# Kernel optimization log

Hardware: AMD Instinct MI355X
Metric: run time of the kernel (lower is better)

The kernel has to match this reference:

```python
import jax, jax.numpy as jnp
import numpy as np

N, E, G = 100000, 3200000, 128
F, H = 9, 64


def _lin(key, fan_in, fan_out):
    s = 1.0 / np.sqrt(fan_in)
    k1, k2 = jax.random.split(key)
    W = jax.random.uniform(k1, (fan_in, fan_out), minval=-s, maxval=s, dtype=jnp.float32)
    b = jax.random.uniform(k2, (fan_out,), minval=-s, maxval=s, dtype=jnp.float32)
    return W, b


def setup_inputs() -> dict:
    key = jax.random.key(0)
    ks = jax.random.split(key, 16)
    x = jax.random.normal(ks[0], (N, F), dtype=jnp.float32)
    edge_index = jax.random.randint(ks[1], (2, E), 0, N, dtype=jnp.int64)
    edge_attr = jax.random.normal(ks[2], (E, 1), dtype=jnp.float32)
    batch = jnp.sort(jax.random.randint(ks[3], (N,), 0, G, dtype=jnp.int64))
    B_total = jax.random.uniform(ks[4], (G,), dtype=jnp.float32)
    terminal_mask = jax.random.randint(ks[5], (N,), 0, 2, dtype=jnp.int32)
    c_cost = jax.random.uniform(ks[6], (N,), dtype=jnp.float32)
    We1, be1 = _lin(ks[7], 1, F)   # GINEConv edge projection edge_dim->in_channels
    W1a, b1a = _lin(ks[8], F, H)
    W1b, b1b = _lin(ks[9], H, H)
    We2, be2 = _lin(ks[10], 1, H)
    W2a, b2a = _lin(ks[11], H, H)
    W2b, b2b = _lin(ks[12], H, H)
    Wr1, br1 = _lin(ks[13], H, H // 2)
    Wr2, br2 = _lin(ks[14], H // 2, 1)
    return dict(x=x, edge_index=edge_index, edge_attr=edge_attr, batch=batch,
                B_total=B_total, terminal_mask=terminal_mask, c_cost=c_cost,
                We1=We1, be1=be1, W1a=W1a, b1a=b1a, W1b=W1b, b1b=b1b,
                We2=We2, be2=be2, W2a=W2a, b2a=b2a, W2b=W2b, b2b=b2b,
                Wr1=Wr1, br1=br1, Wr2=Wr2, br2=br2)


def _gine_conv(h, src, dst, edge_attr, We, be, Wa, ba, Wb, bb):
    # GINEConv (eps=0): nn((1+eps)*x_i + sum_j ReLU(x_j + Lin(edge_attr)))
    ea = edge_attr @ We + be                      # [E, dim]
    msg = jax.nn.relu(h[src] + ea)                # gather + edge fuse + relu
    agg = jax.ops.segment_sum(msg, dst, num_segments=N)  # scatter-add
    z = h + agg
    z = jax.nn.relu(z @ Wa + ba)
    return jax.nn.relu(z @ Wb + bb)


def reference(x, edge_index, edge_attr, batch, B_total, terminal_mask, c_cost,
              We1, be1, W1a, b1a, W1b, b1b, We2, be2, W2a, b2a, W2b, b2b,
              Wr1, br1, Wr2, br2):
    src, dst = edge_index[0], edge_index[1]
    h = _gine_conv(x, src, dst, edge_attr, We1, be1, W1a, b1a, W1b, b1b)
    h = _gine_conv(h, src, dst, edge_attr, We2, be2, W2a, b2a, W2b, b2b)
    pi_raw = jax.nn.sigmoid(jax.nn.relu(h @ Wr1 + br1) @ Wr2 + br2)[:, 0]  # [N]
    pi_raw = pi_raw * (1.0 - terminal_mask.astype(pi_raw.dtype))
    node_expenses = pi_raw * c_cost
    total_expenses = jax.ops.segment_sum(node_expenses, batch, num_segments=B_total.shape[0])
    ratio = jnp.minimum(B_total[batch] / (total_expenses[batch] + 1e-12), 1.0)
    return pi_raw * ratio
```

## Files before the change

### kernel.cpp

```cpp
#include <hip/hip_runtime.h>
#include <hip/hip_fp16.h>
#include <math.h>

#define TPB 256
#define P_BLOCKS 512
#define BSHIFT 8
#define BINS_MAX 512

struct alignas(8)  h2x2 { __half2 a, b; };
struct alignas(16) h2x4 { __half2 a, b, c, d; };

typedef _Float16 f16;
typedef __attribute__((ext_vector_type(8))) _Float16 f16x8;
typedef __attribute__((ext_vector_type(4))) float f32x4;

#define MFMA16(a, b, c) __builtin_amdgcn_mfma_f32_16x16x32_f16(a, b, c, 0, 0, 0)

__global__ void __launch_bounds__(256) k_bhist(const int* __restrict__ dst,
                                               int* __restrict__ counts, int E, int B) {
  __shared__ int h[BINS_MAX];
  int t = threadIdx.x, blk = blockIdx.x;
  for (int i = t; i < B; i += TPB) h[i] = 0;
  __syncthreads();
  int chunk = (E + P_BLOCKS - 1) / P_BLOCKS;
  int s = blk * chunk, e = min(E, s + chunk);
  for (int i = s + t; i < e; i += TPB)
    atomicAdd(&h[__builtin_nontemporal_load(&dst[i]) >> BSHIFT], 1);
  __syncthreads();
  for (int i = t; i < B; i += TPB) counts[i * P_BLOCKS + blk] = h[i];
}

__global__ void k_scan_block(const int* __restrict__ deg, int* __restrict__ offs,
                             int* __restrict__ bsums, int n) {
  __shared__ int lds[256];
  int t = threadIdx.x, b = blockIdx.x;
  int base = b * 1024 + t * 4;
  int v0 = (base + 0 < n) ? deg[base + 0] : 0;
  int v1 = (base + 1 < n) ? deg[base + 1] : 0;
  int v2 = (base + 2 < n) ? deg[base + 2] : 0;
  int v3 = (base + 3 < n) ? deg[base + 3] : 0;
  int s = v0 + v1 + v2 + v3;
  lds[t] = s;
  __syncthreads();
  int acc = s;
  for (int off = 1; off < 256; off <<= 1) {
    int x = (t >= off) ? lds[t - off] : 0;
    __syncthreads();
    acc += x;
    lds[t] = acc;
    __syncthreads();
  }
  int excl = acc - s;
  if (base + 0 < n) offs[base + 0] = excl;
  if (base + 1 < n) offs[base + 1] = excl + v0;
  if (base + 2 < n) offs[base + 2] = excl + v0 + v1;
  if (base + 3 < n) offs[base + 3] = excl + v0 + v1 + v2;
  if (t == 255) bsums[b] = acc;
}

__global__ void k_scan_mid(int* __restrict__ bsums, int nb) {
  __shared__ int lds[256];
  int t = threadIdx.x;
  int v = (t < nb) ? bsums[t] : 0;
  lds[t] = v;
  __syncthreads();
  int acc = v;
  for (int off = 1; off < 256; off <<= 1) {
    int x = (t >= off) ? lds[t - off] : 0;
    __syncthreads();
    acc += x;
    lds[t] = acc;
    __syncthreads();
  }
  if (t < nb) bsums[t] = acc - v;
}

__global__ void k_scan_add(int* __restrict__ offs, const int* __restrict__ bsums,
                           int n, int total) {
  int t = threadIdx.x, b = blockIdx.x;
  int add = bsums[b];
  int base = b * 1024 + t * 4;
#pragma unroll
  for (int j = 0; j < 4; ++j)
    if (base + j < n) offs[base + j] += add;
  if (b == 0 && t == 0) offs[n] = total;
}

__global__ void __launch_bounds__(256) k_bfill(const int* __restrict__ src,
                                               const int* __restrict__ dst,
                                               const float* __restrict__ attr,
                                               const int* __restrict__ offs,
                                               int2* __restrict__ ebuf, int E, int B) {
  __shared__ int cur[BINS_MAX];
  int t = threadIdx.x, blk = blockIdx.x;
  for (int i = t; i < B; i += TPB) cur[i] = offs[i * P_BLOCKS + blk];
  __syncthreads();
  int chunk = (E + P_BLOCKS - 1) / P_BLOCKS;
  int s = blk * chunk, e = min(E, s + chunk);
#pragma unroll 4
  for (int i = s + t; i < e; i += TPB) {
    int d = __builtin_nontemporal_load(&dst[i]);
    int sv = __builtin_nontemporal_load(&src[i]);
    float av = __builtin_nontemporal_load(&attr[i]);
    int bin = d >> BSHIFT;
    int pos = atomicAdd(&cur[bin], 1);
    ebuf[pos] = make_int2((sv << BSHIFT) | (d & ((1 << BSHIFT) - 1)), __float_as_int(av));
  }
}

__global__ void __launch_bounds__(256) k_bsort(const long long* __restrict__ ebuf,
                                               const int* __restrict__ offs,
                                               int2* __restrict__ csr,
                                               int* __restrict__ noffs,
                                               int N, int E) {
  __shared__ int hist[256];
  __shared__ int cursor[256];
  __shared__ int sc[256];
  int t = threadIdx.x, bkt = blockIdx.x;
  hist[t] = 0;
  __syncthreads();
  int s = offs[bkt * P_BLOCKS], e = offs[(bkt + 1) * P_BLOCKS];
#pragma unroll 4
  for (int i = s + t; i < e; i += TPB) {
    long long pv = __builtin_nontemporal_load(&ebuf[i]);
    int key = (int)(unsigned int)(pv & 0xffffffffLL);
    atomicAdd(&hist[key & 255], 1);
  }
  __syncthreads();
  int v = hist[t];
  int acc = v;
  sc[t] = v;
  __syncthreads();
  for (int off = 1; off < 256; off <<= 1) {
    int x = (t >= off) ? sc[t - off] : 0;
    __syncthreads();
    acc += x;
    sc[t] = acc;
    __syncthreads();
  }
  int base = s + acc - v;
  cursor[t] = base;
  int n = (bkt << BSHIFT) + t;
  if (n < N) noffs[n] = base;
  if (bkt == 0 && t == 0) noffs[N] = E;
  __syncthreads();
#pragma unroll 4
  for (int i = s + t; i < e; i += TPB) {
    long long pv = __builtin_nontemporal_load(&ebuf[i]);
    int key = (int)(unsigned int)(pv & 0xffffffffLL);
    int attr = (int)(unsigned int)(((unsigned long long)pv) >> 32);
    int pos = atomicAdd(&cursor[key & 255], 1);
    csr[pos] = make_int2(((unsigned int)key) >> BSHIFT, attr);
  }
}

__global__ void __launch_bounds__(256) k_agg1(
    const float* __restrict__ x, const int2* __restrict__ csr,
    const int* __restrict__ noffs, const float* __restrict__ We1,
    const float* __restrict__ be1, float* __restrict__ u1, int N) {
  int t = blockIdx.x * TPB + threadIdx.x;
  int node = t >> 4, f = t & 15;
  if (node >= N || f >= 9) return;
  int o0 = noffs[node], o1 = noffs[node + 1];
  float we = We1[f], be = be1[f];
  float acc = 0.f;
  int last = o1 - 1;
  for (int e = o0; e < o1; e += 8) {
    int i0 = e;     bool m0 = i0 < o1; i0 = m0 ? i0 : last;
    int i1 = e + 1; bool m1 = i1 < o1; i1 = m1 ? i1 : last;
    int i2 = e + 2; bool m2 = i2 < o1; i2 = m2 ? i2 : last;
    int i3 = e + 3; bool m3 = i3 < o1; i3 = m3 ? i3 : last;
    int i4 = e + 4; bool m4 = i4 < o1; i4 = m4 ? i4 : last;
    int i5 = e + 5; bool m5 = i5 < o1; i5 = m5 ? i5 : last;
    int i6 = e + 6; bool m6 = i6 < o1; i6 = m6 ? i6 : last;
    int i7 = e + 7; bool m7 = i7 < o1; i7 = m7 ? i7 : last;
    int2 p0 = csr[i0], p1 = csr[i1], p2 = csr[i2], p3 = csr[i3];
    int2 p4 = csr[i4], p5 = csr[i5], p6 = csr[i6], p7 = csr[i7];
    float v0 = x[p0.x * 9 + f] + fmaf(__int_as_float(p0.y), we, be);
    float v1 = x[p1.x * 9 + f] + fmaf(__int_as_float(p1.y), we, be);
    float v2 = x[p2.x * 9 + f] + fmaf(__int_as_float(p2.y), we, be);
    float v3 = x[p3.x * 9 + f] + fmaf(__int_as_float(p3.y), we, be);
    float v4 = x[p4.x * 9 + f] + fmaf(__int_as_float(p4.y), we, be);
    float v5 = x[p5.x * 9 + f] + fmaf(__int_as_float(p5.y), we, be);
    float v6 = x[p6.x * 9 + f] + fmaf(__int_as_float(p6.y), we, be);
    float v7 = x[p7.x * 9 + f] + fmaf(__int_as_float(p7.y), we, be);
    acc += m0 ? fmaxf(v0, 0.f) : 0.f;
    acc += m1 ? fmaxf(v1, 0.f) : 0.f;
    acc += m2 ? fmaxf(v2, 0.f) : 0.f;
    acc += m3 ? fmaxf(v3, 0.f) : 0.f;
    acc += m4 ? fmaxf(v4, 0.f) : 0.f;
    acc += m5 ? fmaxf(v5, 0.f) : 0.f;
    acc += m6 ? fmaxf(v6, 0.f) : 0.f;
    acc += m7 ? fmaxf(v7, 0.f) : 0.f;
  }
  u1[node * 9 + f] = x[node * 9 + f] + acc;
}

__global__ void __launch_bounds__(256) k_agg2(
    const __half* __restrict__ h1, const long long* __restrict__ csr,
    const int* __restrict__ noffs, const float* __restrict__ We2,
    const float* __restrict__ be2, float* __restrict__ u2, int N) {
  int gt = blockIdx.x * TPB + threadIdx.x;
  int node = gt >> 6;
  if (node >= N) return;
  int lane = gt & 63;
  int q = lane >> 3, c = lane & 7;
  float4 weA = *(const float4*)&We2[c * 8];
  float4 weB = *(const float4*)&We2[c * 8 + 4];
  float4 beA = *(const float4*)&be2[c * 8];
  float4 beB = *(const float4*)&be2[c * 8 + 4];
  int o0 = noffs[node], o1 = noffs[node + 1];
  float a0 = 0.f, a1 = 0.f, a2 = 0.f, a3 = 0.f, a4 = 0.f, a5 = 0.f, a6 = 0.f, a7 = 0.f;

#define AGG2_ACCM(pv, v, m)                                                  \
  {                                                                          \
    float ea = __int_as_float((int)(unsigned int)(((unsigned long long)(pv)) >> 32)); \
    float2 f0 = __half22float2((v).a), f1 = __half22float2((v).b);           \
    float2 f2 = __half22float2((v).c), f3 = __half22float2((v).d);           \
    a0 += (m) ? fmaxf(f0.x + fmaf(ea, weA.x, beA.x), 0.f) : 0.f;             \
    a1 += (m) ? fmaxf(f0.y + fmaf(ea, weA.y, beA.y), 0.f) : 0.f;             \
    a2 += (m) ? fmaxf(f1.x + fmaf(ea, weA.z, beA.z), 0.f) : 0.f;             \
    a3 += (m) ? fmaxf(f1.y + fmaf(ea, weA.w, beA.w), 0.f) : 0.f;             \
    a4 += (m) ? fmaxf(f2.x + fmaf(ea, weB.x, beB.x), 0.f) : 0.f;             \
    a5 += (m) ? fmaxf(f2.y + fmaf(ea, weB.y, beB.y), 0.f) : 0.f;             \
    a6 += (m) ? fmaxf(f3.x + fmaf(ea, weB.z, beB.z), 0.f) : 0.f;             \
    a7 += (m) ? fmaxf(f3.y + fmaf(ea, weB.w, beB.w), 0.f) : 0.f;             \
  }

  int e = o0;
  if (o1 - e > 32) {
    int last = o1 - 1;
    do {
      long long pv0, pv1, pv2, pv3, pv4, pv5, pv6, pv7;
      bool m0, m1, m2, m3, m4, m5, m6, m7;
      {
        int i0 = e + q;      m0 = i0 < o1; i0 = m0 ? i0 : last;
        int i1 = e + 8 + q;  m1 = i1 < o1; i1 = m1 ? i1 : last;
        int i2 = e + 16 + q; m2 = i2 < o1; i2 = m2 ? i2 : last;
        int i3 = e + 24 + q; m3 = i3 < o1; i3 = m3 ? i3 : last;
        int i4 = e + 32 + q; m4 = i4 < o1; i4 = m4 ? i4 : last;
        int i5 = e + 40 + q; m5 = i5 < o1; i5 = m5 ? i5 : last;
        int i6 = e + 48 + q; m6 = i6 < o1; i6 = m6 ? i6 : last;
        int i7 = e + 56 + q; m7 = i7 < o1; i7 = m7 ? i7 : last;
        pv0 = __builtin_nontemporal_load(&csr[i0]);
        pv1 = __builtin_nontemporal_load(&csr[i1]);
        pv2 = __builtin_nontemporal_load(&csr[i2]);
        pv3 = __builtin_nontemporal_load(&csr[i3]);
        pv4 = __builtin_nontemporal_load(&csr[i4]);
        pv5 = __builtin_nontemporal_load(&csr[i5]);
        pv6 = __builtin_nontemporal_load(&csr[i6]);
        pv7 = __builtin_nontemporal_load(&csr[i7]);
      }
      h2x4 v0 = *(const h2x4*)(h1 + (size_t)(int)(unsigned int)(pv0 & 0xffffffffLL) * 64 + c * 8);
      h2x4 v1 = *(const h2x4*)(h1 + (size_t)(int)(unsigned int)(pv1 & 0xffffffffLL) * 64 + c * 8);
      h2x4 v2 = *(const h2x4*)(h1 + (size_t)(int)(unsigned int)(pv2 & 0xffffffffLL) * 64 + c * 8);
      h2x4 v3 = *(const h2x4*)(h1 + (size_t)(int)(unsigned int)(pv3 & 0xffffffffLL) * 64 + c * 8);
      h2x4 v4 = *(const h2x4*)(h1 + (size_t)(int)(unsigned int)(pv4 & 0xffffffffLL) * 64 + c * 8);
      h2x4 v5 = *(const h2x4*)(h1 + (size_t)(int)(unsigned int)(pv5 & 0xffffffffLL) * 64 + c * 8);
      h2x4 v6 = *(const h2x4*)(h1 + (size_t)(int)(unsigned int)(pv6 & 0xffffffffLL) * 64 + c * 8);
      h2x4 v7 = *(const h2x4*)(h1 + (size_t)(int)(unsigned int)(pv7 & 0xffffffffLL) * 64 + c * 8);
      AGG2_ACCM(pv0, v0, m0); AGG2_ACCM(pv1, v1, m1);
      AGG2_ACCM(pv2, v2, m2); AGG2_ACCM(pv3, v3, m3);
      AGG2_ACCM(pv4, v4, m4); AGG2_ACCM(pv5, v5, m5);
      AGG2_ACCM(pv6, v6, m6); AGG2_ACCM(pv7, v7, m7);
      e += 64;
    } while (o1 - e > 32);
  }
  if (e < o1) {
    int last = o1 - 1;
    int i0 = e + q;      bool m0 = i0 < o1; i0 = m0 ? i0 : last;
    int i1 = e + 8 + q;  bool m1 = i1 < o1; i1 = m1 ? i1 : last;
    int i2 = e + 16 + q; bool m2 = i2 < o1; i2 = m2 ? i2 : last;
    int i3 = e + 24 + q; bool m3 = i3 < o1; i3 = m3 ? i3 : last;
    long long pv0 = __builtin_nontemporal_load(&csr[i0]);
    long long pv1 = __builtin_nontemporal_load(&csr[i1]);
    long long pv2 = __builtin_nontemporal_load(&csr[i2]);
    long long pv3 = __builtin_nontemporal_load(&csr[i3]);
    h2x4 v0 = *(const h2x4*)(h1 + (size_t)(int)(unsigned int)(pv0 & 0xffffffffLL) * 64 + c * 8);
    h2x4 v1 = *(const h2x4*)(h1 + (size_t)(int)(unsigned int)(pv1 & 0xffffffffLL) * 64 + c * 8);
    h2x4 v2 = *(const h2x4*)(h1 + (size_t)(int)(unsigned int)(pv2 & 0xffffffffLL) * 64 + c * 8);
    h2x4 v3 = *(const h2x4*)(h1 + (size_t)(int)(unsigned int)(pv3 & 0xffffffffLL) * 64 + c * 8);
    AGG2_ACCM(pv0, v0, m0); AGG2_ACCM(pv1, v1, m1);
    AGG2_ACCM(pv2, v2, m2); AGG2_ACCM(pv3, v3, m3);
  }
#undef AGG2_ACCM

  a0 += __shfl_xor(a0, 8, 64); a0 += __shfl_xor(a0, 16, 64); a0 += __shfl_xor(a0, 32, 64);
  a1 += __shfl_xor(a1, 8, 64); a1 += __shfl_xor(a1, 16, 64); a1 += __shfl_xor(a1, 32, 64);
  a2 += __shfl_xor(a2, 8, 64); a2 += __shfl_xor(a2, 16, 64); a2 += __shfl_xor(a2, 32, 64);
  a3 += __shfl_xor(a3, 8, 64); a3 += __shfl_xor(a3, 16, 64); a3 += __shfl_xor(a3, 32, 64);
  a4 += __shfl_xor(a4, 8, 64); a4 += __shfl_xor(a4, 16, 64); a4 += __shfl_xor(a4, 32, 64);
  a5 += __shfl_xor(a5, 8, 64); a5 += __shfl_xor(a5, 16, 64); a5 += __shfl_xor(a5, 32, 64);
  a6 += __shfl_xor(a6, 8, 64); a6 += __shfl_xor(a6, 16, 64); a6 += __shfl_xor(a6, 32, 64);
  a7 += __shfl_xor(a7, 8, 64); a7 += __shfl_xor(a7, 16, 64); a7 += __shfl_xor(a7, 32, 64);

  if (q == 0) {
    h2x4 sf = *(const h2x4*)(h1 + (size_t)node * 64 + c * 8);
    float2 s0 = __half22float2(sf.a), s1 = __half22float2(sf.b);
    float2 s2 = __half22float2(sf.c), s3 = __half22float2(sf.d);
    float4 oA, oB;
    oA.x = s0.x + a0; oA.y = s0.y + a1; oA.z = s1.x + a2; oA.w = s1.y + a3;
    oB.x = s2.x + a4; oB.y = s2.y + a5; oB.z = s3.x + a6; oB.w = s3.y + a7;
    *(float4*)&u2[(size_t)node * 64 + c * 8] = oA;
    *(float4*)&u2[(size_t)node * 64 + c * 8 + 4] = oB;
  }
}

__device__ __forceinline__ void splitf8(const float* v, f16x8& h, f16x8& l) {
#pragma unroll
  for (int j = 0; j < 8; ++j) {
    float x = v[j];
    f16 hh = (f16)x;
    h[j] = hh;
    l[j] = (f16)(x - (float)hh);
  }
}

__device__ __forceinline__ void pack_w(const float* __restrict__ W, int Ntiles, int nslots,
                                       f16* hi, f16* lo, int t) {
  int lane = t & 63;
  int kg = lane >> 4, m = lane & 15;
  int Nout = Ntiles * 16;
  for (int s = t >> 6; s < nslots; s += 4) {
    int ks = s / Ntiles, nt = s - ks * Ntiles;
    int kbase = ks * 32 + kg * 8;
    int n = nt * 16 + m;
    float v[8];
#pragma unroll
    for (int j = 0; j < 8; ++j) v[j] = W[(kbase + j) * Nout + n];
    f16x8 h, l;
    splitf8(v, h, l);
    *(f16x8*)&hi[(s * 64 + lane) * 8] = h;
    *(f16x8*)&lo[(s * 64 + lane) * 8] = l;
  }
}

__global__ void __launch_bounds__(256) k_mlp9(
    const float* __restrict__ uin, const float* __restrict__ Wa,
    const float* __restrict__ ba, const float* __restrict__ Wb,
    const float* __restrict__ bb, __half* __restrict__ hout, int N) {
  __shared__ __align__(16) f16 wf1h[2048], wf1l[2048];
  __shared__ __align__(16) f16 wf2h[4096], wf2l[4096];
  __shared__ float ls_z[64 * 65];
  __shared__ float ls_ba[64], ls_bb[64];
  const int t = threadIdx.x;
  const int n0 = blockIdx.x * 64;
  const int w = t >> 6, lane = t & 63;
  const int m = lane & 15, kg = lane >> 4;

  {
    int s = w;
    int n = s * 16 + m;
    float v[8];
#pragma unroll
    for (int j = 0; j < 8; ++j) {
      int k = kg * 8 + j;
      v[j] = (k < 9) ? Wa[k * 64 + n] : 0.f;
    }
    f16x8 h, l;
    splitf8(v, h, l);
    *(f16x8*)&wf1h[(s * 64 + lane) * 8] = h;
    *(f16x8*)&wf1l[(s * 64 + lane) * 8] = l;
  }
  pack_w(Wb, 4, 8, wf2h, wf2l, t);
  if (t < 64) { ls_ba[t] = ba[t]; ls_bb[t] = bb[t]; }
  __syncthreads();

  int row = min(n0 + w * 16 + m, N - 1);
  float av[8];
#pragma unroll
  for (int j = 0; j < 8; ++j) {
    int k = kg * 8 + j;
    av[j] = (k < 9) ? uin[(size_t)row * 9 + k] : 0.f;
  }
  f16x8 a0h, a0l, a1h, a1l;
  splitf8(av, a0h, a0l);

  f32x4 acc[4];
#pragma unroll
  for (int nt = 0; nt < 4; ++nt) { f32x4 z4 = {0.f, 0.f, 0.f, 0.f}; acc[nt] = z4; }
#pragma unroll
  for (int nt = 0; nt < 4; ++nt) {
    f16x8 bh = *(const f16x8*)&wf1h[(nt * 64 + lane) * 8];
    f16x8 bl = *(const f16x8*)&wf1l[(nt * 64 + lane) * 8];
    acc[nt] = MFMA16(a0h, bh, acc[nt]);
    acc[nt] = MFMA16(a0l, bh, acc[nt]);
    acc[nt] = MFMA16(a0h, bl, acc[nt]);
  }
#pragma unroll
  for (int nt = 0; nt < 4; ++nt)
#pragma unroll
    for (int r = 0; r < 4; ++r)
      ls_z[(w * 16 + kg * 4 + r) * 65 + nt * 16 + m] = fmaxf(acc[nt][r] + ls_ba[nt * 16 + m], 0.f);
  __syncthreads();

  const float* zr = &ls_z[(size_t)(w * 16 + m) * 65 + kg * 8];
  {
    float zv0[8], zv1[8];
#pragma unroll
    for (int j = 0; j < 8; ++j) { zv0[j] = zr[j]; zv1[j] = zr[32 + j]; }
    splitf8(zv0, a0h, a0l);
    splitf8(zv1, a1h, a1l);
  }
#pragma unroll
  for (int nt = 0; nt < 4; ++nt) { f32x4 z4 = {0.f, 0.f, 0.f, 0.f}; acc[nt] = z4; }
#pragma unroll
  for (int nt = 0; nt < 4; ++nt) {
#pragma unroll
    for (int ks = 0; ks < 2; ++ks) {
      int s = ks * 4 + nt;
      f16x8 bh = *(const f16x8*)&wf2h[(s * 64 + lane) * 8];
      f16x8 bl = *(const f16x8*)&wf2l[(s * 64 + lane) * 8];
      f16x8 ah = ks ? a1h : a0h;
      f16x8 al = ks ? a1l : a0l;
      acc[nt] = MFMA16(ah, bh, acc[nt]);
      acc[nt] = MFMA16(al, bh, acc[nt]);
      acc[nt] = MFMA16(ah, bl, acc[nt]);
    }
  }
#pragma unroll
  for (int nt = 0; nt < 4; ++nt)
#pragma unroll
    for (int r = 0; r < 4; ++r) {
      int node = n0 + w * 16 + kg * 4 + r;
      if (node < N)
        hout[(size_t)node * 64 + nt * 16 + m] =
            __float2half(fmaxf(acc[nt][r] + ls_bb[nt * 16 + m], 0.f));
    }
}

__global__ void __launch_bounds__(256) k_mlp_ro(
    const float* __restrict__ uin, const float* __restrict__ Wa,
    const float* __restrict__ ba, const float* __restrict__ Wb,
    const float* __restrict__ bb, const float* __restrict__ Wr1,
    const float* __restrict__ br1, const float* __restrict__ Wr2,
    const float* __restrict__ br2, const int* __restrict__ tmask,
    float* __restrict__ pi, int N) {
  __shared__ __align__(16) f16 wf1h[4096], wf1l[4096];
  __shared__ __align__(16) f16 wf2h[4096], wf2l[4096];
  __shared__ __align__(16) f16 wfrh[2048], wfrl[2048];
  __shared__ float ls_z[64 * 65];
  __shared__ float ls_ba[64], ls_bb[64], ls_br1[32], ls_w2[32];
  const int t = threadIdx.x;
  const int n0 = blockIdx.x * 64;

  pack_w(Wa, 4, 8, wf1h, wf1l, t);
  pack_w(Wb, 4, 8, wf2h, wf2l, t);
  pack_w(Wr1, 2, 4, wfrh, wfrl, t);
  if (t < 64) { ls_ba[t] = ba[t]; ls_bb[t] = bb[t]; }
  else if (t < 96) { ls_br1[t - 64] = br1[t - 64]; ls_w2[t - 64] = Wr2[t - 64]; }
  __syncthreads();

  const int w = t >> 6, lane = t & 63;
  const int m = lane & 15, kg = lane >> 4;

  int row = n0 + w * 16 + m;
  row = min(row, N - 1);
  const float* ar = uin + (size_t)row * 64 + kg * 8;
  float av0[8], av1[8];
  {
    f32x4 p0 = *(const f32x4*)ar;
    f32x4 p1 = *(const f32x4*)(ar + 4);
    f32x4 p2 = *(const f32x4*)(ar + 32);
    f32x4 p3 = *(const f32x4*)(ar + 36);
#pragma unroll
    for (int j = 0; j < 4; ++j) {
      av0[j] = p0[j]; av0[4 + j] = p1[j];
      av1[j] = p2[j]; av1[4 + j] = p3[j];
    }
  }
  f16x8 a0h, a0l, a1h, a1l;
  splitf8(av0, a0h, a0l);
  splitf8(av1, a1h, a1l);

  f32x4 acc[4];
#pragma unroll
  for (int nt = 0; nt < 4; ++nt) { f32x4 z4 = {0.f, 0.f, 0.f, 0.f}; acc[nt] = z4; }
#pragma unroll
  for (int nt = 0; nt < 4; ++nt) {
#pragma unroll
    for (int ks = 0; ks < 2; ++ks) {
      int s = ks * 4 + nt;
      f16x8 bh = *(const f16x8*)&wf1h[(s * 64 + lane) * 8];
      f16x8 bl = *(const f16x8*)&wf1l[(s * 64 + lane) * 8];
      f16x8 ah = ks ? a1h : a0h;
      f16x8 al = ks ? a1l : a0l;
      acc[nt] = MFMA16(ah, bh, acc[nt]);
      acc[nt] = MFMA16(al, bh, acc[nt]);
      acc[nt] = MFMA16(ah, bl, acc[nt]);
    }
  }
#pragma unroll
  for (int nt = 0; nt < 4; ++nt)
#pragma unroll
    for (int r = 0; r < 4; ++r)
      ls_z[(w * 16 + kg * 4 + r) * 65 + nt * 16 + m] = fmaxf(acc[nt][r] + ls_ba[nt * 16 + m], 0.f);
  __syncthreads();

  const float* zr = &ls_z[(size_t)(w * 16 + m) * 65 + kg * 8];
  {
    float zv0[8], zv1[8];
#pragma unroll
    for (int j = 0; j < 8; ++j) { zv0[j] = zr[j]; zv1[j] = zr[32 + j]; }
    splitf8(zv0, a0h, a0l);
    splitf8(zv1, a1h, a1l);
  }
#pragma unroll
  for (int nt = 0; nt < 4; ++nt) { f32x4 z4 = {0.f, 0.f, 0.f, 0.f}; acc[nt] = z4; }
#pragma unroll
  for (int nt = 0; nt < 4; ++nt) {
#pragma unroll
    for (int ks = 0; ks < 2; ++ks) {
      int s = ks * 4 + nt;
      f16x8 bh = *(const f16x8*)&wf2h[(s * 64 + lane) * 8];
      f16x8 bl = *(const f16x8*)&wf2l[(s * 64 + lane) * 8];
      f16x8 ah = ks ? a1h : a0h;
      f16x8 al = ks ? a1l : a0l;
      acc[nt] = MFMA16(ah, bh, acc[nt]);
      acc[nt] = MFMA16(al, bh, acc[nt]);
      acc[nt] = MFMA16(ah, bl, acc[nt]);
    }
  }
  __syncthreads();
#pragma unroll
  for (int nt = 0; nt < 4; ++nt)
#pragma unroll
    for (int r = 0; r < 4; ++r)
      ls_z[(w * 16 + kg * 4 + r) * 65 + nt * 16 + m] = fmaxf(acc[nt][r] + ls_bb[nt * 16 + m], 0.f);
  __syncthreads();

  {
    float zv0[8], zv1[8];
#pragma unroll
    for (int j = 0; j < 8; ++j) { zv0[j] = zr[j]; zv1[j] = zr[32 + j]; }
    splitf8(zv0, a0h, a0l);
    splitf8(zv1, a1h, a1l);
  }
  f32x4 accr[2];
#pragma unroll
  for (int nt = 0; nt < 2; ++nt) { f32x4 z4 = {0.f, 0.f, 0.f, 0.f}; accr[nt] = z4; }
#pragma unroll
  for (int nt = 0; nt < 2; ++nt) {
#pragma unroll
    for (int ks = 0; ks < 2; ++ks) {
      int s = ks * 2 + nt;
      f16x8 bh = *(const f16x8*)&wfrh[(s * 64 + lane) * 8];
      f16x8 bl = *(const f16x8*)&wfrl[(s * 64 + lane) * 8];
      f16x8 ah = ks ? a1h : a0h;
      f16x8 al = ks ? a1l : a0l;
      accr[nt] = MFMA16(ah, bh, accr[nt]);
      accr[nt] = MFMA16(al, bh, accr[nt]);
      accr[nt] = MFMA16(ah, bl, accr[nt]);
    }
  }
  float b2 = br2[0];
#pragma unroll
  for (int r = 0; r < 4; ++r) {
    float v0 = fmaxf(accr[0][r] + ls_br1[m], 0.f) * ls_w2[m];
    float v1 = fmaxf(accr[1][r] + ls_br1[16 + m], 0.f) * ls_w2[16 + m];
    float tr = v0 + v1;
    tr += __shfl_xor(tr, 1, 64);
    tr += __shfl_xor(tr, 2, 64);
    tr += __shfl_xor(tr, 4, 64);
    tr += __shfl_xor(tr, 8, 64);
    if (m == 0) {
      int node = n0 + w * 16 + kg * 4 + r;
      if (node < N) {
        float sg = 1.f / (1.f + expf(-(tr + b2)));
        pi[node] = sg * (1.f - (float)tmask[node]);
      }
    }
  }
}

__global__ void k_grpsum(const float* __restrict__ pi, const float* __restrict__ c_cost,
                         const int* __restrict__ batch, float* __restrict__ exp_tot, int N) {
  __shared__ float lsf[256];
  __shared__ int lsi[256];
  int t = threadIdx.x;
  int i = blockIdx.x * TPB + t;
  bool valid = i < N;
  int g = valid ? batch[i] : 0;
  float v = valid ? pi[i] * c_cost[i] : 0.f;
  lsi[t] = valid ? g : 0x7fffffff;
  __syncthreads();
  for (int s = 128; s > 0; s >>= 1) { if (t < s) lsi[t] = min(lsi[t], lsi[t + s]); __syncthreads(); }
  int gmin = lsi[0];
  __syncthreads();
  lsi[t] = valid ? g : -1;
  __syncthreads();
  for (int s = 128; s > 0; s >>= 1) { if (t < s) lsi[t] = max(lsi[t], lsi[t + s]); __syncthreads(); }
  int gmax = lsi[0];
  __syncthreads();
  for (int gg = gmin; gg <= gmax; ++gg) {
    lsf[t] = (valid && g == gg) ? v : 0.f;
    __syncthreads();
    for (int s = 128; s > 0; s >>= 1) { if (t < s) lsf[t] += lsf[t + s]; __syncthreads(); }
    if (t == 0) atomicAdd(&exp_tot[gg], lsf[0]);
    __syncthreads();
  }
}

__global__ void k_final(const float* __restrict__ pi, const int* __restrict__ batch,
                        const float* __restrict__ B_total, const float* __restrict__ exp_tot,
                        float* __restrict__ out, int N) {
  int i = blockIdx.x * TPB + threadIdx.x;
  if (i < N) {
    int g = batch[i];
    float ratio = fminf(B_total[g] / (exp_tot[g] + 1e-12f), 1.f);
    out[i] = pi[i] * ratio;
  }
}

extern "C" void kernel_launch(void* const* d_in, const int* in_sizes, int n_in,
                              void* d_out, int out_size, void* d_ws, size_t ws_size,
                              hipStream_t stream) {
  const float* x     = (const float*)d_in[0];
  const int*   ei    = (const int*)d_in[1];
  const float* eattr = (const float*)d_in[2];
  const int*   batch = (const int*)d_in[3];
  const float* Btot  = (const float*)d_in[4];
  const int*   tmask = (const int*)d_in[5];
  const float* ccost = (const float*)d_in[6];
  const float* We1 = (const float*)d_in[7],  *be1 = (const float*)d_in[8];
  const float* W1a = (const float*)d_in[9],  *b1a = (const float*)d_in[10];
  const float* W1b = (const float*)d_in[11], *b1b = (const float*)d_in[12];
  const float* We2 = (const float*)d_in[13], *be2 = (const float*)d_in[14];
  const float* W2a = (const float*)d_in[15], *b2a = (const float*)d_in[16];
  const float* W2b = (const float*)d_in[17], *b2b = (const float*)d_in[18];
  const float* Wr1 = (const float*)d_in[19], *br1 = (const float*)d_in[20];
  const float* Wr2 = (const float*)d_in[21], *br2 = (const float*)d_in[22];
  float* out = (float*)d_out;

  const int N = in_sizes[0] / 9;
  const int E = in_sizes[2];
  const int G = in_sizes[4];
  const int* src = ei;
  const int* dst = ei + E;
  const int B = (N + (1 << BSHIFT) - 1) >> BSHIFT;
  const int nscan = B * P_BLOCKS;

  size_t cur = 0;
  auto alloc = [&](size_t elems) { size_t r = cur; cur += elems; cur = (cur + 63) & ~(size_t)63; return r; };
  char* wsb = (char*)d_ws;
  size_t o_exp    = alloc(G);
  size_t o_counts = alloc(nscan);
  size_t o_offs   = alloc(nscan + 1);
  size_t o_bsums  = alloc(256);
  size_t o_noffs  = alloc(N + 1);
  size_t o_csr    = alloc(2 * (size_t)E);
  size_t e_or_h   = (2 * (size_t)E > (size_t)N * 32) ? 2 * (size_t)E : (size_t)N * 32;
  size_t o_ebuf   = alloc(e_or_h);
  size_t o_u1     = alloc((size_t)N * 9);
  size_t o_u2     = alloc((size_t)N * 64);
  size_t o_pi     = alloc(N);
  (void)ws_size;

  float* exp_t  = (float*)wsb + o_exp;
  int*   counts = (int*)wsb + o_counts;
  int*   offs   = (int*)wsb + o_offs;
  int*   bsums  = (int*)wsb + o_bsums;
  int*   noffs  = (int*)wsb + o_noffs;
  int2*  csr    = (int2*)((int*)wsb + o_csr);
  int2*  ebuf   = (int2*)((int*)wsb + o_ebuf);
  __half* h1h   = (__half*)((int*)wsb + o_ebuf);
  float* u1     = (float*)wsb + o_u1;
  float* u2     = (float*)wsb + o_u2;
  float* pi     = (float*)wsb + o_pi;

  (void)hipMemsetAsync(exp_t, 0, (size_t)G * 4, stream);

  const int nb = (nscan + 1023) / 1024;

  k_bhist<<<P_BLOCKS, TPB, 0, stream>>>(dst, counts, E, B);
  k_scan_block<<<nb, TPB, 0, stream>>>(counts, offs, bsums, nscan);
  k_scan_mid<<<1, 256, 0, stream>>>(bsums, nb);
  k_scan_add<<<nb, TPB, 0, stream>>>(offs, bsums, nscan, E);
  k_bfill<<<P_BLOCKS, TPB, 0, stream>>>(src, dst, eattr, offs, ebuf, E, B);
  k_bsort<<<B, TPB, 0, stream>>>((const long long*)ebuf, offs, csr, noffs, N, E);

  k_agg1<<<((size_t)N * 16 + TPB - 1) / TPB, TPB, 0, stream>>>(x, csr, noffs, We1, be1, u1, N);
  k_mlp9<<<(N + 63) / 64, TPB, 0, stream>>>(u1, W1a, b1a, W1b, b1b, h1h, N);

  k_agg2<<<((size_t)N * 64 + TPB - 1) / TPB, TPB, 0, stream>>>(h1h, (const long long*)csr, noffs, We2, be2, u2, N);
  k_mlp_ro<<<(N + 63) / 64, TPB, 0, stream>>>(u2, W2a, b2a, W2b, b2b, Wr1, br1, Wr2, br2, tmask, pi, N);

  k_grpsum<<<(N + TPB - 1) / TPB, TPB, 0, stream>>>(pi, ccost, batch, exp_t, N);
  k_final<<<(N + TPB - 1) / TPB, TPB, 0, stream>>>(pi, batch, Btot, exp_t, out, N);
}
```

Before: 408.8 us.

## Replace two-pass bucket sort CSR build with direct global-atomic counting sort

Replaces the bucketed histogram, bucket fill and per-bucket LDS sort with a per-node global atomic histogram, a scan over N node counts, and a single fill pass that places each edge through a global atomicAdd on its destination's cursor. This removes the intermediate edge buffer pass and the second sort kernel. In exchange it uses millions of global atomics on random addresses and makes the order of edges within each node nondeterministic, which changes the order of float summation.

```diff
diff --git a/kernel.cpp b/kernel.cpp
--- a/kernel.cpp
+++ b/kernel.cpp
@@ -3,9 +3,6 @@
 #include <math.h>
 
 #define TPB 256
-#define P_BLOCKS 512
-#define BSHIFT 8
-#define BINS_MAX 512
 
 struct alignas(8)  h2x2 { __half2 a, b; };
 struct alignas(16) h2x4 { __half2 a, b, c, d; };
@@ -16,18 +13,11 @@
 
 #define MFMA16(a, b, c) __builtin_amdgcn_mfma_f32_16x16x32_f16(a, b, c, 0, 0, 0)
 
-__global__ void __launch_bounds__(256) k_bhist(const int* __restrict__ dst,
-                                               int* __restrict__ counts, int E, int B) {
-  __shared__ int h[BINS_MAX];
-  int t = threadIdx.x, blk = blockIdx.x;
-  for (int i = t; i < B; i += TPB) h[i] = 0;
-  __syncthreads();
-  int chunk = (E + P_BLOCKS - 1) / P_BLOCKS;
-  int s = blk * chunk, e = min(E, s + chunk);
-  for (int i = s + t; i < e; i += TPB)
-    atomicAdd(&h[__builtin_nontemporal_load(&dst[i]) >> BSHIFT], 1);
-  __syncthreads();
-  for (int i = t; i < B; i += TPB) counts[i * P_BLOCKS + blk] = h[i];
+__global__ void __launch_bounds__(256) k_nhist(const int* __restrict__ dst,
+                                               int* __restrict__ counts, int E) {
+  int stride = gridDim.x * TPB;
+  for (int i = blockIdx.x * TPB + threadIdx.x; i < E; i += stride)
+    atomicAdd(&counts[__builtin_nontemporal_load(&dst[i])], 1);
 }
 
 __global__ void k_scan_block(const int* __restrict__ deg, int* __restrict__ offs,
@@ -86,71 +76,19 @@
   if (b == 0 && t == 0) offs[n] = total;
 }
 
-__global__ void __launch_bounds__(256) k_bfill(const int* __restrict__ src,
-                                               const int* __restrict__ dst,
-                                               const float* __restrict__ attr,
-                                               const int* __restrict__ offs,
-                                               int2* __restrict__ ebuf, int E, int B) {
-  __shared__ int cur[BINS_MAX];
-  int t = threadIdx.x, blk = blockIdx.x;
-  for (int i = t; i < B; i += TPB) cur[i] = offs[i * P_BLOCKS + blk];
-  __syncthreads();
-  int chunk = (E + P_BLOCKS - 1) / P_BLOCKS;
-  int s = blk * chunk, e = min(E, s + chunk);
-#pragma unroll 4
-  for (int i = s + t; i < e; i += TPB) {
+__global__ void __launch_bounds__(256) k_fill(const int* __restrict__ src,
+                                              const int* __restrict__ dst,
+                                              const float* __restrict__ attr,
+                                              const int* __restrict__ noffs,
+                                              int* __restrict__ cnt,
+                                              int2* __restrict__ csr, int E) {
+  int stride = gridDim.x * TPB;
+  for (int i = blockIdx.x * TPB + threadIdx.x; i < E; i += stride) {
     int d = __builtin_nontemporal_load(&dst[i]);
     int sv = __builtin_nontemporal_load(&src[i]);
     float av = __builtin_nontemporal_load(&attr[i]);
-    int bin = d >> BSHIFT;
-    int pos = atomicAdd(&cur[bin], 1);
-    ebuf[pos] = make_int2((sv << BSHIFT) | (d & ((1 << BSHIFT) - 1)), __float_as_int(av));
-  }
-}
-
-__global__ void __launch_bounds__(256) k_bsort(const long long* __restrict__ ebuf,
-                                               const int* __restrict__ offs,
-                                               int2* __restrict__ csr,
-                                               int* __restrict__ noffs,
-                                               int N, int E) {
-  __shared__ int hist[256];
-  __shared__ int cursor[256];
-  __shared__ int sc[256];
-  int t = threadIdx.x, bkt = blockIdx.x;
-  hist[t] = 0;
-  __syncthreads();
-  int s = offs[bkt * P_BLOCKS], e = offs[(bkt + 1) * P_BLOCKS];
-#pragma unroll 4
-  for (int i = s + t; i < e; i += TPB) {
-    long long pv = __builtin_nontemporal_load(&ebuf[i]);
-    int key = (int)(unsigned int)(pv & 0xffffffffLL);
-    atomicAdd(&hist[key & 255], 1);
-  }
-  __syncthreads();
-  int v = hist[t];
-  int acc = v;
-  sc[t] = v;
-  __syncthreads();
-  for (int off = 1; off < 256; off <<= 1) {
-    int x = (t >= off) ? sc[t - off] : 0;
-    __syncthreads();
-    acc += x;
-    sc[t] = acc;
-    __syncthreads();
-  }
-  int base = s + acc - v;
-  cursor[t] = base;
-  int n = (bkt << BSHIFT) + t;
-  if (n < N) noffs[n] = base;
-  if (bkt == 0 && t == 0) noffs[N] = E;
-  __syncthreads();
-#pragma unroll 4
-  for (int i = s + t; i < e; i += TPB) {
-    long long pv = __builtin_nontemporal_load(&ebuf[i]);
-    int key = (int)(unsigned int)(pv & 0xffffffffLL);
-    int attr = (int)(unsigned int)(((unsigned long long)pv) >> 32);
-    int pos = atomicAdd(&cursor[key & 255], 1);
-    csr[pos] = make_int2(((unsigned int)key) >> BSHIFT, attr);
+    int pos = noffs[d] + atomicAdd(&cnt[d], 1);
+    csr[pos] = make_int2(sv, __float_as_int(av));
   }
 }
 
@@ -637,20 +575,17 @@
   const int G = in_sizes[4];
   const int* src = ei;
   const int* dst = ei + E;
-  const int B = (N + (1 << BSHIFT) - 1) >> BSHIFT;
-  const int nscan = B * P_BLOCKS;
 
   size_t cur = 0;
   auto alloc = [&](size_t elems) { size_t r = cur; cur += elems; cur = (cur + 63) & ~(size_t)63; return r; };
   char* wsb = (char*)d_ws;
   size_t o_exp    = alloc(G);
-  size_t o_counts = alloc(nscan);
-  size_t o_offs   = alloc(nscan + 1);
+  size_t o_counts = alloc(N);
+  size_t o_cnt    = alloc(N);
+  size_t o_noffs  = alloc(N + 1);
   size_t o_bsums  = alloc(256);
-  size_t o_noffs  = alloc(N + 1);
   size_t o_csr    = alloc(2 * (size_t)E);
-  size_t e_or_h   = (2 * (size_t)E > (size_t)N * 32) ? 2 * (size_t)E : (size_t)N * 32;
-  size_t o_ebuf   = alloc(e_or_h);
+  size_t o_h1     = alloc((size_t)N * 32);
   size_t o_u1     = alloc((size_t)N * 9);
   size_t o_u2     = alloc((size_t)N * 64);
   size_t o_pi     = alloc(N);
@@ -658,26 +593,26 @@
 
   float* exp_t  = (float*)wsb + o_exp;
   int*   counts = (int*)wsb + o_counts;
-  int*   offs   = (int*)wsb + o_offs;
+  int*   cnt    = (int*)wsb + o_cnt;
+  int*   noffs  = (int*)wsb + o_noffs;
   int*   bsums  = (int*)wsb + o_bsums;
-  int*   noffs  = (int*)wsb + o_noffs;
   int2*  csr    = (int2*)((int*)wsb + o_csr);
-  int2*  ebuf   = (int2*)((int*)wsb + o_ebuf);
-  __half* h1h   = (__half*)((int*)wsb + o_ebuf);
+  __half* h1h   = (__half*)((int*)wsb + o_h1);
   float* u1     = (float*)wsb + o_u1;
   float* u2     = (float*)wsb + o_u2;
   float* pi     = (float*)wsb + o_pi;
 
   (void)hipMemsetAsync(exp_t, 0, (size_t)G * 4, stream);
-
-  const int nb = (nscan + 1023) / 1024;
-
-  k_bhist<<<P_BLOCKS, TPB, 0, stream>>>(dst, counts, E, B);
-  k_scan_block<<<nb, TPB, 0, stream>>>(counts, offs, bsums, nscan);
+  (void)hipMemsetAsync(counts, 0, (size_t)N * 4, stream);
+  (void)hipMemsetAsync(cnt, 0, (size_t)N * 4, stream);
+
+  const int nb = (N + 1023) / 1024;
+
+  k_nhist<<<1024, TPB, 0, stream>>>(dst, counts, E);
+  k_scan_block<<<nb, TPB, 0, stream>>>(counts, noffs, bsums, N);
   k_scan_mid<<<1, 256, 0, stream>>>(bsums, nb);
-  k_scan_add<<<nb, TPB, 0, stream>>>(offs, bsums, nscan, E);
-  k_bfill<<<P_BLOCKS, TPB, 0, stream>>>(src, dst, eattr, offs, ebuf, E, B);
-  k_bsort<<<B, TPB, 0, stream>>>((const long long*)ebuf, offs, csr, noffs, N, E);
+  k_scan_add<<<nb, TPB, 0, stream>>>(noffs, bsums, N, E);
+  k_fill<<<2048, TPB, 0, stream>>>(src, dst, eattr, noffs, cnt, csr, E);
 
   k_agg1<<<((size_t)N * 16 + TPB - 1) / TPB, TPB, 0, stream>>>(x, csr, noffs, We1, be1, u1, N);
   k_mlp9<<<(N + 63) / 64, TPB, 0, stream>>>(u1, W1a, b1a, W1b, b1b, h1h, N);
```

After: 565.7 us. 38.4% more time.
